# Performance work log

Measured on AMD Instinct MI355X. Metric: run time of the kernel, lower is better.

## Reference

```python
import jax, jax.numpy as jnp
import numpy as np
import math

EMSIZE = 1024
B, S = 4, 1024
N = B * S

def setup_inputs() -> dict:
    key = jax.random.key(0)
    k1, k2, k3, k4, k5 = jax.random.split(key, 5)
    x = jax.random.normal(k1, (B, S, EMSIZE), dtype=jnp.float32)
    mask = jax.random.randint(k2, (N, N), 0, 2, dtype=jnp.int32)
    # nn.Linear default init scale ~ 1/sqrt(fan_in); use small normal weights
    sc = 1.0 / math.sqrt(EMSIZE)
    Wq = jax.random.normal(k3, (EMSIZE, EMSIZE), dtype=jnp.float32) * sc
    Wk = jax.random.normal(k4, (EMSIZE, EMSIZE), dtype=jnp.float32) * sc
    Wv = jax.random.normal(k5, (EMSIZE, EMSIZE), dtype=jnp.float32) * sc
    return {"x": x, "mask": mask, "Wq": Wq, "Wk": Wk, "Wv": Wv}

def reference(x, mask, Wq, Wk, Wv):
    b, s, e = x.shape
    xf = x.reshape(b * s, e)                       # [N, E]
    q = xf @ Wq.T                                  # nn.Linear: x @ W^T
    k = xf @ Wk.T
    v = xf @ Wv.T
    sim = q @ k.T                                  # [N, N] full cross-batch scores
    sim = jnp.where(mask == 0, jnp.float32(-1e20), sim)
    # NOTE: original scales AFTER masking, matching masked_fill then divide
    attn = jax.nn.softmax(sim / math.sqrt(e), axis=-1)
    out = attn @ v                                 # [N, E]
    return out.reshape(b, s, e)
```

## Files before the change

kernel.cpp:

```cpp
#include <hip/hip_runtime.h>
#include <hip/hip_bf16.h>
#include <math.h>


typedef __attribute__((ext_vector_type(8))) __bf16 bf16x8;
typedef __attribute__((ext_vector_type(4))) __bf16 bf16x4;
typedef __attribute__((ext_vector_type(4))) float f32x4;

__device__ __forceinline__ void gload_lds16(const void* g, void* l) {
  __builtin_amdgcn_global_load_lds(
      (__attribute__((address_space(1))) void*)(g),
      (__attribute__((address_space(3))) void*)(l), 16, 0, 0);
}

#define WAITB(N) asm volatile("s_waitcnt vmcnt(" #N ")\ns_barrier" ::: "memory")
#define BAR()    asm volatile("s_barrier" ::: "memory")

__global__ __launch_bounds__(256) void cvt_all(const float* __restrict__ x,
                                               const float* __restrict__ wq,
                                               const float* __restrict__ wk,
                                               const float* __restrict__ wv,
                                               __bf16* __restrict__ xb,
                                               __bf16* __restrict__ wqb,
                                               __bf16* __restrict__ wkb,
                                               __bf16* __restrict__ wvb) {
  int b = blockIdx.x;
  const float* in;
  __bf16* out;
  int base;
  if (b < 4096)      { in = x;  out = xb;  base = b; }
  else if (b < 5120) { in = wq; out = wqb; base = b - 4096; }
  else if (b < 6144) { in = wk; out = wkb; base = b - 5120; }
  else               { in = wv; out = wvb; base = b - 6144; }
  int i = base * 256 + threadIdx.x;
  float4 f = ((const float4*)in)[i];
  bf16x4 o;
  o[0] = (__bf16)f.x; o[1] = (__bf16)f.y; o[2] = (__bf16)f.z; o[3] = (__bf16)f.w;
  ((bf16x4*)out)[i] = o;
}


#define GEMM_PROLOGUE_DB()                                \
  __shared__ __bf16 lsA[2][128 * 64];                     \
  __shared__ __bf16 lsB[2][128 * 64];                     \
  const int tid = threadIdx.x;                            \
  const int lane = tid & 63;                              \
  const int w = tid >> 6;                                 \
  const int wr = w >> 1, wc = w & 1;                      \
  const int hi = lane >> 4;                               \
  const int lo = lane & 15;                               \
  f32x4 acc[4][4] = {};

#define GEMM_STAGE(buf, Aptr, lda, Bptr, ldb, k0)                          \
  {                                                                        \
    _Pragma("unroll") for (int i = 0; i < 4; ++i) {                        \
      int c = i * 256 + tid;                                               \
      int r = c >> 3, cv = c & 7;                                          \
      gload_lds16((Aptr) + (row0 + r) * (long)(lda) + (k0) + cv * 8,       \
                  lsA[buf] + (i * 256 + w * 64) * 8);                      \
    }                                                                      \
    _Pragma("unroll") for (int i = 0; i < 4; ++i) {                        \
      int c = i * 256 + tid;                                               \
      int r = c >> 3, cv = c & 7;                                          \
      gload_lds16((Bptr) + (col0 + r) * (long)(ldb) + (k0) + cv * 8,       \
                  lsB[buf] + (i * 256 + w * 64) * 8);                      \
    }                                                                      \
  }

#define GEMM_COMPUTE(buf)                                                  \
  _Pragma("unroll") for (int kk = 0; kk < 64; kk += 32) {                  \
    bf16x8 af[4], bfr[4];                                                  \
    _Pragma("unroll") for (int m = 0; m < 4; ++m)                          \
      af[m] = *(const bf16x8*)(lsA[buf] + (wr * 64 + m * 16 + lo) * 64 + kk + hi * 8); \
    _Pragma("unroll") for (int n = 0; n < 4; ++n)                          \
      bfr[n] = *(const bf16x8*)(lsB[buf] + (wc * 64 + n * 16 + lo) * 64 + kk + hi * 8); \
    _Pragma("unroll") for (int m = 0; m < 4; ++m)                          \
      _Pragma("unroll") for (int n = 0; n < 4; ++n)                        \
        acc[m][n] = __builtin_amdgcn_mfma_f32_16x16x32_bf16(af[m], bfr[n], acc[m][n], 0, 0, 0); \
  }

#define GEMM_MAINLOOP_P2(Aptr, lda, Bptr, ldb, kstart, kend)               \
  GEMM_STAGE(0, Aptr, lda, Bptr, ldb, (kstart));                           \
  GEMM_STAGE(1, Aptr, lda, Bptr, ldb, (kstart) + 64);                      \
  {                                                                        \
    int cur = 0;                                                           \
    for (int k0 = (kstart); k0 < (kend); k0 += 64) {                       \
      if (k0 + 64 < (kend)) { WAITB(8); } else { WAITB(0); }               \
      GEMM_COMPUTE(cur);                                                   \
      BAR();                                                               \
      if (k0 + 128 < (kend))                                               \
        GEMM_STAGE(cur, Aptr, lda, Bptr, ldb, k0 + 128);                   \
      cur ^= 1;                                                            \
    }                                                                      \
  }

__global__ __launch_bounds__(256) void qk_gemm(const __bf16* __restrict__ A,
                                               const __bf16* __restrict__ B,
                                               __bf16* __restrict__ C) {
  const int raw = blockIdx.x;
  const int wid = (raw & 7) * 128 + (raw >> 3);
  const long row0 = (long)(wid >> 5) * 128;
  const long col0 = (long)(wid & 31) * 128;
  GEMM_PROLOGUE_DB();
  GEMM_MAINLOOP_P2(A, 1024, B, 1024, 0, 1024);
#pragma unroll
  for (int m = 0; m < 4; ++m)
#pragma unroll
    for (int n = 0; n < 4; ++n)
#pragma unroll
      for (int i = 0; i < 4; ++i) {
        long r = row0 + wr * 64 + m * 16 + hi * 4 + i;
        long cc = col0 + wc * 64 + n * 16 + lo;
        C[r * 4096 + cc] = (__bf16)acc[m][n][i];
      }
}

__global__ __launch_bounds__(256) void qkv_gemm(const __bf16* __restrict__ xb,
                                                const __bf16* __restrict__ wq,
                                                const __bf16* __restrict__ wk,
                                                const __bf16* __restrict__ wv,
                                                __bf16* __restrict__ qb,
                                                __bf16* __restrict__ kb,
                                                __bf16* __restrict__ vtb) {
  const int raw = blockIdx.x;
  const int wid = (raw & 7) * 96 + (raw >> 3);
  const int z = wid >> 8;
  const int r2 = wid & 255;
  const long row0 = (long)(r2 >> 3) * 128;
  const long col0 = (long)(r2 & 7) * 128;
  const __bf16* Bw = (z == 0) ? wq : (z == 1) ? wk : wv;
  GEMM_PROLOGUE_DB();
  GEMM_MAINLOOP_P2(xb, 1024, Bw, 1024, 0, 1024);
#pragma unroll
  for (int m = 0; m < 4; ++m)
#pragma unroll
    for (int n = 0; n < 4; ++n)
#pragma unroll
      for (int i = 0; i < 4; ++i) {
        long r = row0 + wr * 64 + m * 16 + hi * 4 + i;
        long cc = col0 + wc * 64 + n * 16 + lo;
        __bf16 v = (__bf16)acc[m][n][i];
        if (z == 0)      qb[r * 1024 + cc] = v;
        else if (z == 1) kb[r * 1024 + cc] = v;
        else             vtb[cc * 4096 + r] = v;
      }
}

__global__ __launch_bounds__(256) void pv_gemm(const __bf16* __restrict__ attn,
                                               const __bf16* __restrict__ vt,
                                               float* __restrict__ out,
                                               float* __restrict__ p1) {
  const int raw = blockIdx.x;
  const int wid = (raw & 7) * 64 + (raw >> 3);
  const int z = wid >> 8;
  const int r2 = wid & 255;
  const long row0 = (long)(r2 >> 3) * 128;
  const long col0 = (long)(r2 & 7) * 128;
  float* C = z ? p1 : out;
  const int kbase = z * 2048;
  GEMM_PROLOGUE_DB();
  GEMM_MAINLOOP_P2(attn, 4096, vt, 4096, kbase, kbase + 2048);
#pragma unroll
  for (int m = 0; m < 4; ++m)
#pragma unroll
    for (int n = 0; n < 4; ++n)
#pragma unroll
      for (int i = 0; i < 4; ++i) {
        long r = row0 + wr * 64 + m * 16 + hi * 4 + i;
        long cc = col0 + wc * 64 + n * 16 + lo;
        C[r * 1024 + cc] = acc[m][n][i];
      }
}

__global__ __launch_bounds__(256) void reduce_add(float* __restrict__ out,
                                                  const float* __restrict__ p1) {
  int i = blockIdx.x * 256 + threadIdx.x;
  float4 a = ((const float4*)out)[i];
  float4 b = ((const float4*)p1)[i];
  a.x += b.x; a.y += b.y; a.z += b.z; a.w += b.w;
  ((float4*)out)[i] = a;
}

__global__ __launch_bounds__(256) void softmax_rows(__bf16* __restrict__ sim,
                                                    const int* __restrict__ mask) {
  const int row = blockIdx.x;
  __bf16* rp = sim + (size_t)row * 4096;
  const int4* mrow = (const int4*)(mask + (size_t)row * 4096);
  const int tid = threadIdx.x;

  float vals[16];
  float lmax = -INFINITY;
#pragma unroll
  for (int j = 0; j < 2; ++j) {
    bf16x8 s = ((const bf16x8*)rp)[tid + 256 * j];
    int4 m0 = mrow[(tid + 256 * j) * 2];
    int4 m1 = mrow[(tid + 256 * j) * 2 + 1];
    float f[8];
#pragma unroll
    for (int e = 0; e < 8; ++e) f[e] = (float)s[e];
    f[0] = m0.x ? f[0] : -1e20f;  f[1] = m0.y ? f[1] : -1e20f;
    f[2] = m0.z ? f[2] : -1e20f;  f[3] = m0.w ? f[3] : -1e20f;
    f[4] = m1.x ? f[4] : -1e20f;  f[5] = m1.y ? f[5] : -1e20f;
    f[6] = m1.z ? f[6] : -1e20f;  f[7] = m1.w ? f[7] : -1e20f;
#pragma unroll
    for (int e = 0; e < 8; ++e) {
      vals[8 * j + e] = f[e];
      lmax = fmaxf(lmax, f[e]);
    }
  }
#pragma unroll
  for (int off = 32; off; off >>= 1) lmax = fmaxf(lmax, __shfl_xor(lmax, off));
  __shared__ float red[4];
  __shared__ float bro[2];
  if ((tid & 63) == 0) red[tid >> 6] = lmax;
  __syncthreads();
  if (tid == 0) bro[0] = fmaxf(fmaxf(red[0], red[1]), fmaxf(red[2], red[3]));
  __syncthreads();
  const float m = bro[0];

  float e[16];
  float lsum = 0.f;
#pragma unroll
  for (int j = 0; j < 16; ++j) {
    e[j] = __expf((vals[j] - m) * 0.03125f);
    lsum += e[j];
  }
#pragma unroll
  for (int off = 32; off; off >>= 1) lsum += __shfl_xor(lsum, off);
  if ((tid & 63) == 0) red[tid >> 6] = lsum;
  __syncthreads();
  if (tid == 0) bro[1] = red[0] + red[1] + red[2] + red[3];
  __syncthreads();
  const float inv = 1.0f / bro[1];

#pragma unroll
  for (int j = 0; j < 2; ++j) {
    bf16x8 o;
#pragma unroll
    for (int q = 0; q < 8; ++q) o[q] = (__bf16)(e[8 * j + q] * inv);
    ((bf16x8*)rp)[tid + 256 * j] = o;
  }
}

extern "C" void kernel_launch(void* const* d_in, const int* in_sizes, int n_in,
                              void* d_out, int out_size, void* d_ws, size_t ws_size,
                              hipStream_t stream) {
  const float* x = (const float*)d_in[0];
  const int* mask = (const int*)d_in[1];
  const float* Wq = (const float*)d_in[2];
  const float* Wk = (const float*)d_in[3];
  const float* Wv = (const float*)d_in[4];
  float* out = (float*)d_out;

  char* ws = (char*)d_ws;
  __bf16* wqb = (__bf16*)(ws);
  __bf16* wkb = (__bf16*)(ws + (2ull << 20));
  __bf16* wvb = (__bf16*)(ws + (4ull << 20));
  __bf16* xb  = (__bf16*)(ws + (6ull << 20));
  __bf16* qb  = (__bf16*)(ws + (14ull << 20));
  __bf16* kb  = (__bf16*)(ws + (22ull << 20));
  __bf16* vtb = (__bf16*)(ws + (30ull << 20));
  __bf16* sim = (__bf16*)(ws + (38ull << 20));
  float*  p1  = (float*)(ws);

  cvt_all<<<7168, 256, 0, stream>>>(x, Wq, Wk, Wv, xb, wqb, wkb, wvb);

  dim3 blk(256);
  qkv_gemm<<<768, blk, 0, stream>>>(xb, wqb, wkb, wvb, qb, kb, vtb);
  qk_gemm<<<1024, blk, 0, stream>>>(qb, kb, sim);
  softmax_rows<<<4096, 256, 0, stream>>>(sim, mask);
  pv_gemm<<<512, blk, 0, stream>>>(sim, vtb, out, p1);
  reduce_add<<<4096, 256, 0, stream>>>(out, p1);
}
```

Measured before the change: 190.6 us.

## Switch GEMMs to 256x256 tiles with 8 waves, swizzled LDS and 4-way split-K

Replaces the three 128x128 GEMM kernels (256 threads) with 256x256-tile kernels using 512 threads, each wave owning a 128x64 sub-tile. LDS loads use an XOR swizzle to avoid bank conflicts. The MFMA phases are interleaved with barriers and s_setprio. The PV GEMM is split four ways along K instead of two, with a 4-input reduction, and the workspace is relaid out to hold the extra partial buffers. The aim is more data reuse per tile and less LDS conflict. The cost is fewer blocks (192-256 across the chip's CUs), more barriers, and extra partial-sum traffic.

Measured after the change: 196.7 us. 1.03x slower.

```diff
diff --git a/kernel.cpp b/kernel.cpp
--- a/kernel.cpp
+++ b/kernel.cpp
@@ -15,6 +15,185 @@
 
 #define WAITB(N) asm volatile("s_waitcnt vmcnt(" #N ")\ns_barrier" ::: "memory")
 #define BAR()    asm volatile("s_barrier" ::: "memory")
+
+__device__ __forceinline__ void g8_stage(const __bf16* __restrict__ src, long ld,
+                                         long r0, int k0, __bf16* dst, int tid) {
+#pragma unroll
+  for (int j = 0; j < 4; ++j) {
+    int p = tid + j * 512;
+    int row = p >> 3;
+    int cg = (p & 7) ^ (row & 7);
+    gload_lds16(src + (r0 + row) * ld + k0 + cg * 8, dst + p * 8);
+  }
+}
+
+#define LDA8(sAc, kkc)                                                        \
+  _Pragma("unroll") for (int m = 0; m < 8; ++m) {                             \
+    int r = wr * 128 + m * 16 + lo;                                           \
+    af[m] = *(const bf16x8*)((sAc) + r * 64 + (((hi + ((kkc) >> 3)) ^ (lo & 7)) * 8)); \
+  }
+#define LDB2(sBc, kkc, nh)                                                    \
+  _Pragma("unroll") for (int n = 0; n < 2; ++n) {                             \
+    int r = wc * 64 + ((nh)*2 + n) * 16 + lo;                                 \
+    bf2[n] = *(const bf16x8*)((sBc) + r * 64 + (((hi + ((kkc) >> 3)) ^ (lo & 7)) * 8)); \
+  }
+#define MM(nh)                                                                \
+  __builtin_amdgcn_s_setprio(1);                                              \
+  _Pragma("unroll") for (int m = 0; m < 8; ++m)                               \
+    _Pragma("unroll") for (int n = 0; n < 2; ++n)                             \
+      acc[m][(nh)*2 + n] = __builtin_amdgcn_mfma_f32_16x16x32_bf16(           \
+          af[m], bf2[n], acc[m][(nh)*2 + n], 0, 0, 0);                        \
+  __builtin_amdgcn_s_setprio(0);
+
+__device__ __forceinline__ void g8_loop(const __bf16* __restrict__ A, long lda, long row0,
+                                        const __bf16* __restrict__ B, long ldb, long col0,
+                                        int kstart, __bf16* sA, __bf16* sB,
+                                        f32x4 (&acc)[8][4], int tid) {
+  const int lane = tid & 63, w = tid >> 6;
+  const int wr = w >> 2, wc = w & 3;
+  const int lo = lane & 15, hi = lane >> 4;
+  const int NT = 16;
+
+  g8_stage(A, lda, row0, kstart, sA, tid);
+  g8_stage(B, ldb, col0, kstart, sB, tid);
+  g8_stage(A, lda, row0, kstart + 64, sA + 16384, tid);
+  g8_stage(B, ldb, col0, kstart + 64, sB + 16384, tid);
+  WAITB(8);
+
+  for (int t = 0; t < NT; ++t) {
+    const int d = t & 1;
+    const __bf16* sAc = sA + d * 16384;
+    const __bf16* sBc = sB + d * 16384;
+    bf16x8 af[8], bf2[2];
+    LDA8(sAc, 0); LDB2(sBc, 0, 0);
+    BAR(); MM(0); BAR();
+    LDB2(sBc, 0, 1);
+    BAR(); MM(1); BAR();
+    LDA8(sAc, 32); LDB2(sBc, 32, 0);
+    BAR(); MM(0); BAR();
+    LDB2(sBc, 32, 1);
+    BAR(); MM(1); BAR();
+    if (t + 2 < NT) {
+      g8_stage(A, lda, row0, kstart + (t + 2) * 64, sA + d * 16384, tid);
+      g8_stage(B, ldb, col0, kstart + (t + 2) * 64, sB + d * 16384, tid);
+      WAITB(8);
+    } else {
+      WAITB(0);
+    }
+  }
+}
+
+
+__global__ __launch_bounds__(512) void qkv8(const __bf16* __restrict__ xb,
+                                            const __bf16* __restrict__ wq,
+                                            const __bf16* __restrict__ wk,
+                                            const __bf16* __restrict__ wv,
+                                            __bf16* __restrict__ qb,
+                                            __bf16* __restrict__ kb,
+                                            __bf16* __restrict__ vtb) {
+  __shared__ __bf16 sA[2 * 16384];
+  __shared__ __bf16 sB[2 * 16384];
+  const int raw = blockIdx.x;
+  const int wid = (raw & 7) * 24 + (raw >> 3);
+  const int z = wid >> 6;
+  const int r2 = wid & 63;
+  const long row0 = (long)(r2 >> 2) * 256;
+  const long col0 = (long)(r2 & 3) * 256;
+  const __bf16* Bw = (z == 0) ? wq : (z == 1) ? wk : wv;
+  f32x4 acc[8][4] = {};
+  g8_loop(xb, 1024, row0, Bw, 1024, col0, 0, sA, sB, acc, threadIdx.x);
+
+  const int lane = threadIdx.x & 63, w = threadIdx.x >> 6;
+  const int wr = w >> 2, wc = w & 3;
+  const int lo = lane & 15, hi = lane >> 4;
+#pragma unroll
+  for (int m = 0; m < 8; ++m)
+#pragma unroll
+    for (int n = 0; n < 4; ++n)
+#pragma unroll
+      for (int i = 0; i < 4; ++i) {
+        long r = row0 + wr * 128 + m * 16 + hi * 4 + i;
+        long c = col0 + wc * 64 + n * 16 + lo;
+        __bf16 v = (__bf16)acc[m][n][i];
+        if (z == 0)      qb[r * 1024 + c] = v;
+        else if (z == 1) kb[r * 1024 + c] = v;
+        else             vtb[c * 4096 + r] = v;
+      }
+}
+
+__global__ __launch_bounds__(512) void qk8(const __bf16* __restrict__ qb,
+                                           const __bf16* __restrict__ kb,
+                                           __bf16* __restrict__ sim) {
+  __shared__ __bf16 sA[2 * 16384];
+  __shared__ __bf16 sB[2 * 16384];
+  const int raw = blockIdx.x;
+  const int wid = (raw & 7) * 32 + (raw >> 3);
+  const long row0 = (long)(wid >> 4) * 256;
+  const long col0 = (long)(wid & 15) * 256;
+  f32x4 acc[8][4] = {};
+  g8_loop(qb, 1024, row0, kb, 1024, col0, 0, sA, sB, acc, threadIdx.x);
+
+  const int lane = threadIdx.x & 63, w = threadIdx.x >> 6;
+  const int wr = w >> 2, wc = w & 3;
+  const int lo = lane & 15, hi = lane >> 4;
+#pragma unroll
+  for (int m = 0; m < 8; ++m)
+#pragma unroll
+    for (int n = 0; n < 4; ++n)
+#pragma unroll
+      for (int i = 0; i < 4; ++i) {
+        long r = row0 + wr * 128 + m * 16 + hi * 4 + i;
+        long c = col0 + wc * 64 + n * 16 + lo;
+        sim[r * 4096 + c] = (__bf16)acc[m][n][i];
+      }
+}
+
+__global__ __launch_bounds__(512) void pv8(const __bf16* __restrict__ attn,
+                                           const __bf16* __restrict__ vt,
+                                           float* __restrict__ out,
+                                           float* __restrict__ p1,
+                                           float* __restrict__ p2,
+                                           float* __restrict__ p3) {
+  __shared__ __bf16 sA[2 * 16384];
+  __shared__ __bf16 sB[2 * 16384];
+  const int raw = blockIdx.x;
+  const int wid = (raw & 7) * 32 + (raw >> 3);
+  const int z = wid >> 6;
+  const int r2 = wid & 63;
+  const long row0 = (long)(r2 >> 2) * 256;
+  const long col0 = (long)(r2 & 3) * 256;
+  float* C = (z == 0) ? out : (z == 1) ? p1 : (z == 2) ? p2 : p3;
+  f32x4 acc[8][4] = {};
+  g8_loop(attn, 4096, row0, vt, 4096, col0, z * 1024, sA, sB, acc, threadIdx.x);
+
+  const int lane = threadIdx.x & 63, w = threadIdx.x >> 6;
+  const int wr = w >> 2, wc = w & 3;
+  const int lo = lane & 15, hi = lane >> 4;
+#pragma unroll
+  for (int m = 0; m < 8; ++m)
+#pragma unroll
+    for (int n = 0; n < 4; ++n)
+#pragma unroll
+      for (int i = 0; i < 4; ++i) {
+        long r = row0 + wr * 128 + m * 16 + hi * 4 + i;
+        long c = col0 + wc * 64 + n * 16 + lo;
+        C[r * 1024 + c] = acc[m][n][i];
+      }
+}
+
+__global__ __launch_bounds__(256) void reduce_add4(float* __restrict__ out,
+                                                   const float* __restrict__ a,
+                                                   const float* __restrict__ b,
+                                                   const float* __restrict__ c) {
+  int i = blockIdx.x * 256 + threadIdx.x;
+  float4 o = ((const float4*)out)[i];
+  float4 x = ((const float4*)a)[i];
+  float4 y = ((const float4*)b)[i];
+  float4 z = ((const float4*)c)[i];
+  o.x += x.x + y.x + z.x; o.y += x.y + y.y + z.y;
+  o.z += x.z + y.z + z.z; o.w += x.w + y.w + z.w;
+  ((float4*)out)[i] = o;
+}
 
 __global__ __launch_bounds__(256) void cvt_all(const float* __restrict__ x,
                                                const float* __restrict__ wq,
@@ -39,148 +218,6 @@
   ((bf16x4*)out)[i] = o;
 }
 
-
-#define GEMM_PROLOGUE_DB()                                \
-  __shared__ __bf16 lsA[2][128 * 64];                     \
-  __shared__ __bf16 lsB[2][128 * 64];                     \
-  const int tid = threadIdx.x;                            \
-  const int lane = tid & 63;                              \
-  const int w = tid >> 6;                                 \
-  const int wr = w >> 1, wc = w & 1;                      \
-  const int hi = lane >> 4;                               \
-  const int lo = lane & 15;                               \
-  f32x4 acc[4][4] = {};
-
-#define GEMM_STAGE(buf, Aptr, lda, Bptr, ldb, k0)                          \
-  {                                                                        \
-    _Pragma("unroll") for (int i = 0; i < 4; ++i) {                        \
-      int c = i * 256 + tid;                                               \
-      int r = c >> 3, cv = c & 7;                                          \
-      gload_lds16((Aptr) + (row0 + r) * (long)(lda) + (k0) + cv * 8,       \
-                  lsA[buf] + (i * 256 + w * 64) * 8);                      \
-    }                                                                      \
-    _Pragma("unroll") for (int i = 0; i < 4; ++i) {                        \
-      int c = i * 256 + tid;                                               \
-      int r = c >> 3, cv = c & 7;                                          \
-      gload_lds16((Bptr) + (col0 + r) * (long)(ldb) + (k0) + cv * 8,       \
-                  lsB[buf] + (i * 256 + w * 64) * 8);                      \
-    }                                                                      \
-  }
-
-#define GEMM_COMPUTE(buf)                                                  \
-  _Pragma("unroll") for (int kk = 0; kk < 64; kk += 32) {                  \
-    bf16x8 af[4], bfr[4];                                                  \
-    _Pragma("unroll") for (int m = 0; m < 4; ++m)                          \
-      af[m] = *(const bf16x8*)(lsA[buf] + (wr * 64 + m * 16 + lo) * 64 + kk + hi * 8); \
-    _Pragma("unroll") for (int n = 0; n < 4; ++n)                          \
-      bfr[n] = *(const bf16x8*)(lsB[buf] + (wc * 64 + n * 16 + lo) * 64 + kk + hi * 8); \
-    _Pragma("unroll") for (int m = 0; m < 4; ++m)                          \
-      _Pragma("unroll") for (int n = 0; n < 4; ++n)                        \
-        acc[m][n] = __builtin_amdgcn_mfma_f32_16x16x32_bf16(af[m], bfr[n], acc[m][n], 0, 0, 0); \
-  }
-
-#define GEMM_MAINLOOP_P2(Aptr, lda, Bptr, ldb, kstart, kend)               \
-  GEMM_STAGE(0, Aptr, lda, Bptr, ldb, (kstart));                           \
-  GEMM_STAGE(1, Aptr, lda, Bptr, ldb, (kstart) + 64);                      \
-  {                                                                        \
-    int cur = 0;                                                           \
-    for (int k0 = (kstart); k0 < (kend); k0 += 64) {                       \
-      if (k0 + 64 < (kend)) { WAITB(8); } else { WAITB(0); }               \
-      GEMM_COMPUTE(cur);                                                   \
-      BAR();                                                               \
-      if (k0 + 128 < (kend))                                               \
-        GEMM_STAGE(cur, Aptr, lda, Bptr, ldb, k0 + 128);                   \
-      cur ^= 1;                                                            \
-    }                                                                      \
-  }
-
-__global__ __launch_bounds__(256) void qk_gemm(const __bf16* __restrict__ A,
-                                               const __bf16* __restrict__ B,
-                                               __bf16* __restrict__ C) {
-  const int raw = blockIdx.x;
-  const int wid = (raw & 7) * 128 + (raw >> 3);
-  const long row0 = (long)(wid >> 5) * 128;
-  const long col0 = (long)(wid & 31) * 128;
-  GEMM_PROLOGUE_DB();
-  GEMM_MAINLOOP_P2(A, 1024, B, 1024, 0, 1024);
-#pragma unroll
-  for (int m = 0; m < 4; ++m)
-#pragma unroll
-    for (int n = 0; n < 4; ++n)
-#pragma unroll
-      for (int i = 0; i < 4; ++i) {
-        long r = row0 + wr * 64 + m * 16 + hi * 4 + i;
-        long cc = col0 + wc * 64 + n * 16 + lo;
-        C[r * 4096 + cc] = (__bf16)acc[m][n][i];
-      }
-}
-
-__global__ __launch_bounds__(256) void qkv_gemm(const __bf16* __restrict__ xb,
-                                                const __bf16* __restrict__ wq,
-                                                const __bf16* __restrict__ wk,
-                                                const __bf16* __restrict__ wv,
-                                                __bf16* __restrict__ qb,
-                                                __bf16* __restrict__ kb,
-                                                __bf16* __restrict__ vtb) {
-  const int raw = blockIdx.x;
-  const int wid = (raw & 7) * 96 + (raw >> 3);
-  const int z = wid >> 8;
-  const int r2 = wid & 255;
-  const long row0 = (long)(r2 >> 3) * 128;
-  const long col0 = (long)(r2 & 7) * 128;
-  const __bf16* Bw = (z == 0) ? wq : (z == 1) ? wk : wv;
-  GEMM_PROLOGUE_DB();
-  GEMM_MAINLOOP_P2(xb, 1024, Bw, 1024, 0, 1024);
-#pragma unroll
-  for (int m = 0; m < 4; ++m)
-#pragma unroll
-    for (int n = 0; n < 4; ++n)
-#pragma unroll
-      for (int i = 0; i < 4; ++i) {
-        long r = row0 + wr * 64 + m * 16 + hi * 4 + i;
-        long cc = col0 + wc * 64 + n * 16 + lo;
-        __bf16 v = (__bf16)acc[m][n][i];
-        if (z == 0)      qb[r * 1024 + cc] = v;
-        else if (z == 1) kb[r * 1024 + cc] = v;
-        else             vtb[cc * 4096 + r] = v;
-      }
-}
-
-__global__ __launch_bounds__(256) void pv_gemm(const __bf16* __restrict__ attn,
-                                               const __bf16* __restrict__ vt,
-                                               float* __restrict__ out,
-                                               float* __restrict__ p1) {
-  const int raw = blockIdx.x;
-  const int wid = (raw & 7) * 64 + (raw >> 3);
-  const int z = wid >> 8;
-  const int r2 = wid & 255;
-  const long row0 = (long)(r2 >> 3) * 128;
-  const long col0 = (long)(r2 & 7) * 128;
-  float* C = z ? p1 : out;
-  const int kbase = z * 2048;
-  GEMM_PROLOGUE_DB();
-  GEMM_MAINLOOP_P2(attn, 4096, vt, 4096, kbase, kbase + 2048);
-#pragma unroll
-  for (int m = 0; m < 4; ++m)
-#pragma unroll
-    for (int n = 0; n < 4; ++n)
-#pragma unroll
-      for (int i = 0; i < 4; ++i) {
-        long r = row0 + wr * 64 + m * 16 + hi * 4 + i;
-        long cc = col0 + wc * 64 + n * 16 + lo;
-        C[r * 1024 + cc] = acc[m][n][i];
-      }
-}
-
-__global__ __launch_bounds__(256) void reduce_add(float* __restrict__ out,
-                                                  const float* __restrict__ p1) {
-  int i = blockIdx.x * 256 + threadIdx.x;
-  float4 a = ((const float4*)out)[i];
-  float4 b = ((const float4*)p1)[i];
-  a.x += b.x; a.y += b.y; a.z += b.z; a.w += b.w;
-  ((float4*)out)[i] = a;
-}
-
 __global__ __launch_bounds__(256) void softmax_rows(__bf16* __restrict__ sim,
                                                     const int* __restrict__ mask) {
   const int row = blockIdx.x;
@@ -253,22 +290,24 @@
   float* out = (float*)d_out;
 
   char* ws = (char*)d_ws;
-  __bf16* wqb = (__bf16*)(ws);
-  __bf16* wkb = (__bf16*)(ws + (2ull << 20));
-  __bf16* wvb = (__bf16*)(ws + (4ull << 20));
-  __bf16* xb  = (__bf16*)(ws + (6ull << 20));
-  __bf16* qb  = (__bf16*)(ws + (14ull << 20));
-  __bf16* kb  = (__bf16*)(ws + (22ull << 20));
-  __bf16* vtb = (__bf16*)(ws + (30ull << 20));
+  __bf16* vtb = (__bf16*)(ws);
+  __bf16* xb  = (__bf16*)(ws + (8ull << 20));
+  __bf16* wqb = (__bf16*)(ws + (16ull << 20));
+  __bf16* wkb = (__bf16*)(ws + (18ull << 20));
+  __bf16* wvb = (__bf16*)(ws + (20ull << 20));
+  __bf16* qb  = (__bf16*)(ws + (22ull << 20));
+  __bf16* kb  = (__bf16*)(ws + (30ull << 20));
   __bf16* sim = (__bf16*)(ws + (38ull << 20));
-  float*  p1  = (float*)(ws);
+  float*  p1  = (float*)(ws + (8ull << 20));
+  float*  p2  = (float*)(ws + (70ull << 20));
+  float*  p3  = (float*)(ws + (86ull << 20));
 
   cvt_all<<<7168, 256, 0, stream>>>(x, Wq, Wk, Wv, xb, wqb, wkb, wvb);
 
-  dim3 blk(256);
-  qkv_gemm<<<768, blk, 0, stream>>>(xb, wqb, wkb, wvb, qb, kb, vtb);
-  qk_gemm<<<1024, blk, 0, stream>>>(qb, kb, sim);
+  dim3 blk(512);
+  qkv8<<<192, blk, 0, stream>>>(xb, wqb, wkb, wvb, qb, kb, vtb);
+  qk8<<<256, blk, 0, stream>>>(qb, kb, sim);
   softmax_rows<<<4096, 256, 0, stream>>>(sim, mask);
-  pv_gemm<<<512, blk, 0, stream>>>(sim, vtb, out, p1);
-  reduce_add<<<4096, 256, 0, stream>>>(out, p1);
-}
+  pv8<<<256, blk, 0, stream>>>(sim, vtb, out, p1, p2, p3);
+  reduce_add4<<<4096, 256, 0, stream>>>(out, p1, p2, p3);
+}
```
